# Optimization experiments

Measured on AMD Instinct MI355X. Metric: run time of the kernel, lower is better.

Reference implementation:

```python
import jax, jax.numpy as jnp
import numpy as np

E, S, Q, NN_NODES, R = 2048, 256, 25, 36, 15
H = 128  # MLP hidden width


def setup_inputs() -> dict:
    key = jax.random.key(0)
    ks = jax.random.split(key, 16)
    g = lambda k, shape, scale=1.0: (jax.random.normal(k, shape, dtype=jnp.float32) * scale)
    inp = {
        "nodes": g(ks[0], (E, NN_NODES, 2)),
        "W1": g(ks[1], (2, H), 1.0 / np.sqrt(2.0)),
        "b1": jnp.zeros((H,), jnp.float32),
        "W2": g(ks[2], (H, H), 1.0 / np.sqrt(H)),
        "b2": jnp.zeros((H,), jnp.float32),
        "W3": g(ks[3], (H, H), 1.0 / np.sqrt(H)),
        "b3": jnp.zeros((H,), jnp.float32),
        "W4": g(ks[4], (H, 1), 1.0 / np.sqrt(H)),
        "b4": jnp.zeros((1,), jnp.float32),
        # 2nd-derivative interpolation matrices of the inter basis B at the
        # sub-element quadrature points (shared across big elements).
        "Ixx": g(ks[5], (S, Q, NN_NODES), 0.1),
        "Iyy": g(ks[6], (S, Q, NN_NODES), 0.1),
        # per-big-element 2x2 Hessian change-of-coordinates map (B_DD_inter)
        "B_DD": g(ks[7], (E, 2, 2)),
        "w_quad": jax.random.uniform(ks[8], (Q,), dtype=jnp.float32),
        # test-function values at quadrature points (b.Base)
        "Base": g(ks[9], (Q, R)),
        # per-sub-element Jacobians and precomputed RHS projections F_total
        "J": jax.random.uniform(ks[10], (E, S), dtype=jnp.float32),
        "F": g(ks[11], (E, S, R)),
    }
    return inp


def _mlp(x, W1, b1, W2, b2, W3, b3, W4, b4):
    h = jnp.tanh(x @ W1 + b1)
    h = jnp.tanh(h @ W2 + b2)
    h = jnp.tanh(h @ W3 + b3)
    return h @ W4 + b4


def reference(nodes, W1, b1, W2, b2, W3, b3, W4, b4,
              Ixx, Iyy, B_DD, w_quad, Base, J, F):
    # NN evaluated once per big element at its interpolation nodes: [E, n_nodes]
    ev = _mlp(nodes.reshape(-1, 2), W1, b1, W2, b2, W3, b3, W4, b4)
    ev = ev.reshape(E, NN_NODES)
    d2x = jnp.einsum("sqn,en->esq", Ixx, ev)
    d2y = jnp.einsum("sqn,en->esq", Iyy, ev)
    grad_second = jnp.stack([d2x, d2y], axis=2)           # [E,S,2,Q]
    # B_DD_inter @ grad_second^T, per big element
    grad_second = jnp.einsum("eij,esjq->esiq", B_DD, grad_second)
    integrand_1 = grad_second.sum(axis=2)                 # [E,S,Q]
    # u_NN_el[r] = -J * sum_q w[q] * Base[q,r] * integrand_1[q]
    u_el = -J[:, :, None] * jnp.einsum("q,qr,esq->esr", w_quad, Base, integrand_1)
    res = u_el - F                                        # [E,S,R]
    # loss_element = mean over test functions, summed over all (big, sub) elements
    return jnp.sum(jnp.mean(jnp.square(res), axis=-1))
```

## Files before the change

### kernel.cpp

```cpp
#include <hip/hip_runtime.h>

#define EN 2048
#define SN 256
#define QN 25
#define NNODES 36
#define RN 15
#define HN 128
#define KP 96
#define NTOT (SN * RN)

typedef __attribute__((ext_vector_type(8))) short short8;
typedef __attribute__((ext_vector_type(4))) float f32x4;
typedef __attribute__((ext_vector_type(2))) unsigned int uint2v;

__device__ __forceinline__ unsigned short f2bf(float f) {
    unsigned int u = __float_as_uint(f);
    u += 0x7fffu + ((u >> 16) & 1u);
    return (unsigned short)(u >> 16);
}
__device__ __forceinline__ float bf2f(unsigned short h) {
    return __uint_as_float(((unsigned int)h) << 16);
}
__device__ __forceinline__ float fast_tanh(float x) {
    float xs = x * 2.885390082f;
    xs = fminf(fmaxf(xs, -60.f), 60.f);
    float e = __builtin_amdgcn_exp2f(xs);
    float r = __builtin_amdgcn_rcpf(e + 1.f);
    return fmaf(-2.f, r, 1.f);
}

__device__ __forceinline__ void load_W(const float* __restrict__ W,
                                       unsigned short (*Ws)[136], int t)
{
    const int n = t & 127;
    const int h = t >> 7;
    #pragma unroll
    for (int kk = 0; kk < 16; kk++) {
        const int k0 = (kk * 2 + h) * 4;
        const float a0 = W[(k0 + 0) * HN + n];
        const float a1 = W[(k0 + 1) * HN + n];
        const float a2 = W[(k0 + 2) * HN + n];
        const float a3 = W[(k0 + 3) * HN + n];
        uint2v pk;
        pk[0] = (unsigned)f2bf(a0) | ((unsigned)f2bf(a1) << 16);
        pk[1] = (unsigned)f2bf(a2) | ((unsigned)f2bf(a3) << 16);
        *(uint2v*)&Ws[n][k0] = pk;
    }
}

__device__ __forceinline__ void mfma_layer(unsigned short (*Hs)[136],
                                           const unsigned short (*Ws)[136],
                                           const float* __restrict__ bias,
                                           int wv, int rowA, int quad)
{
    const int r0 = wv * 32;
    short8 afrag[2][4];
    #pragma unroll
    for (int rt = 0; rt < 2; rt++)
        #pragma unroll
        for (int kt = 0; kt < 4; kt++)
            afrag[rt][kt] = *(const short8*)&Hs[r0 + rt * 16 + rowA][kt * 32 + quad * 8];

    f32x4 acc[2][8];
    const f32x4 zero = {0.f, 0.f, 0.f, 0.f};
    #pragma unroll
    for (int rt = 0; rt < 2; rt++)
        #pragma unroll
        for (int nt = 0; nt < 8; nt++) acc[rt][nt] = zero;

    #pragma unroll
    for (int nt = 0; nt < 8; nt++) {
        #pragma unroll
        for (int kt = 0; kt < 4; kt++) {
            const short8 bfrag = *(const short8*)&Ws[nt * 16 + rowA][kt * 32 + quad * 8];
            acc[0][nt] = __builtin_amdgcn_mfma_f32_16x16x32_bf16(afrag[0][kt], bfrag, acc[0][nt], 0, 0, 0);
            acc[1][nt] = __builtin_amdgcn_mfma_f32_16x16x32_bf16(afrag[1][kt], bfrag, acc[1][nt], 0, 0, 0);
        }
    }
    #pragma unroll
    for (int nt = 0; nt < 8; nt++) {
        const int col = nt * 16 + rowA;
        const float bv = bias[col];
        #pragma unroll
        for (int rt = 0; rt < 2; rt++) {
            #pragma unroll
            for (int rg = 0; rg < 4; rg++) {
                const float v = fast_tanh(acc[rt][nt][rg] + bv);
                Hs[r0 + rt * 16 + quad * 4 + rg][col] = f2bf(v);
            }
        }
    }
}

#define MLP_BLOCKS 576
#define MC_BLOCKS  SN

__global__ __launch_bounds__(256, 2)
void prep_kernel(const float* __restrict__ nodes,
                 const float* __restrict__ W1, const float* __restrict__ b1,
                 const float* __restrict__ W2, const float* __restrict__ b2,
                 const float* __restrict__ W3, const float* __restrict__ b3,
                 const float* __restrict__ W4, const float* __restrict__ b4,
                 const float* __restrict__ B_DD,
                 const float* __restrict__ Ixx, const float* __restrict__ Iyy,
                 const float* __restrict__ wq, const float* __restrict__ Base,
                 unsigned short* __restrict__ evcb,
                 unsigned short* __restrict__ Mcb,
                 float* __restrict__ out)
{
    __shared__ unsigned short Hs[128][136];
    __shared__ unsigned short Ws[128][136];
    __shared__ float WB[QN * 16];
    const int bid = blockIdx.x;
    const int t   = threadIdx.x;

    if (bid < MLP_BLOCKS) {
        const int lane = t & 63;
        const int wv   = t >> 6;
        const int rowA = lane & 15;
        const int quad = lane >> 4;

        {
            const int p  = t >> 1;
            const int P  = bid * 128 + p;
            const float x0 = nodes[2 * P], x1 = nodes[2 * P + 1];
            const int n0 = (t & 1) * 64;
            #pragma unroll
            for (int i = 0; i < 16; i++) {
                const int n = n0 + 4 * i;
                const float4 wa = *(const float4*)(W1 + n);
                const float4 wb = *(const float4*)(W1 + HN + n);
                const float4 bb = *(const float4*)(b1 + n);
                const float h0 = fast_tanh(fmaf(x0, wa.x, fmaf(x1, wb.x, bb.x)));
                const float h1 = fast_tanh(fmaf(x0, wa.y, fmaf(x1, wb.y, bb.y)));
                const float h2 = fast_tanh(fmaf(x0, wa.z, fmaf(x1, wb.z, bb.z)));
                const float h3 = fast_tanh(fmaf(x0, wa.w, fmaf(x1, wb.w, bb.w)));
                uint2v pk;
                pk[0] = (unsigned)f2bf(h0) | ((unsigned)f2bf(h1) << 16);
                pk[1] = (unsigned)f2bf(h2) | ((unsigned)f2bf(h3) << 16);
                *(uint2v*)&Hs[p][n] = pk;
            }
        }
        load_W(W2, Ws, t);
        __syncthreads();
        mfma_layer(Hs, Ws, b2, wv, rowA, quad);
        __syncthreads();
        load_W(W3, Ws, t);
        __syncthreads();
        mfma_layer(Hs, Ws, b3, wv, rowA, quad);
        {
            const int p  = t >> 1;
            const int k0 = (t & 1) * 64;
            float d = 0.f;
            #pragma unroll
            for (int i = 0; i < 8; i++) {
                const short8 h = *(const short8*)&Hs[p][k0 + 8 * i];
                const float4 wA = *(const float4*)(W4 + k0 + 8 * i);
                const float4 wB = *(const float4*)(W4 + k0 + 8 * i + 4);
                d = fmaf(bf2f((unsigned short)h[0]), wA.x, d);
                d = fmaf(bf2f((unsigned short)h[1]), wA.y, d);
                d = fmaf(bf2f((unsigned short)h[2]), wA.z, d);
                d = fmaf(bf2f((unsigned short)h[3]), wA.w, d);
                d = fmaf(bf2f((unsigned short)h[4]), wB.x, d);
                d = fmaf(bf2f((unsigned short)h[5]), wB.y, d);
                d = fmaf(bf2f((unsigned short)h[6]), wB.z, d);
                d = fmaf(bf2f((unsigned short)h[7]), wB.w, d);
            }
            d += __shfl_xor(d, 1, 64);
            if ((t & 1) == 0) {
                const float ev = d + b4[0];
                const int P  = bid * 128 + p;
                const int e  = P / NNODES;
                const int ne = P - e * NNODES;
                const float c0 = B_DD[4 * e + 0] + B_DD[4 * e + 2];
                const float c1 = B_DD[4 * e + 1] + B_DD[4 * e + 3];
                evcb[e * KP + ne]          = f2bf(c0 * ev);
                evcb[e * KP + NNODES + ne] = f2bf(c1 * ev);
                if (ne < KP - 2 * NNODES)
                    evcb[e * KP + 2 * NNODES + ne] = 0;
            }
        }
    } else {
        const int s = bid - MLP_BLOCKS;
        if (s == 0 && t == 0) out[0] = 0.f;
        float* I_lds = (float*)&Hs[0][0];
        for (int i = t; i < QN * 16; i += 256) {
            const int q = i >> 4, r = i & 15;
            if (r < RN) WB[i] = wq[q] * Base[q * RN + r];
        }
        const float* __restrict__ Ia = Ixx + (size_t)s * (QN * NNODES);
        const float* __restrict__ Ib = Iyy + (size_t)s * (QN * NNODES);
        for (int i = t; i < QN * NNODES; i += 256) {
            I_lds[i]               = Ia[i];
            I_lds[QN * NNODES + i] = Ib[i];
        }
        __syncthreads();
        for (int o = t; o < RN * KP; o += 256) {
            const int c = o % KP;
            const int r = o / KP;
            float v = 0.f;
            if (c < 2 * NNODES) {
                const float* __restrict__ Ip =
                    I_lds + ((c < NNODES) ? c : (QN * NNODES + c - NNODES));
                float a0 = 0.f, a1 = 0.f;
                #pragma unroll
                for (int q = 0; q < QN - 1; q += 2) {
                    a0 = fmaf(WB[q * 16 + r],       Ip[q * NNODES],       a0);
                    a1 = fmaf(WB[(q + 1) * 16 + r], Ip[(q + 1) * NNODES], a1);
                }
                a0 = fmaf(WB[(QN - 1) * 16 + r], Ip[(QN - 1) * NNODES], a0);
                v = a0 + a1;
            }
            Mcb[((size_t)s * RN + r) * KP + c] = f2bf(v);
        }
    }
}

__global__ __launch_bounds__(256, 4)
void loss_kernel(const unsigned short* __restrict__ evcb,
                 const unsigned short* __restrict__ Mcb,
                 const float* __restrict__ J, const float* __restrict__ F,
                 float* __restrict__ out)
{
    const int t    = threadIdx.x;
    const int lane = t & 63;
    const int wv   = t >> 6;
    const int rowA = lane & 15;
    const int quad = lane >> 4;
    const int m0 = (blockIdx.x & 31) * 64;
    const int n0 = (blockIdx.x >> 5) * 128 + wv * 32;

    float Fv[2][16];
    #pragma unroll
    for (int nt = 0; nt < 2; nt++) {
        const int n = n0 + nt * 16 + rowA;
        #pragma unroll
        for (int mt = 0; mt < 4; mt++)
            #pragma unroll
            for (int rg = 0; rg < 4; rg++)
                Fv[nt][mt * 4 + rg] = F[(size_t)(m0 + mt * 16 + quad * 4 + rg) * NTOT + n];
    }

    f32x4 acc[4][2];
    const f32x4 zero = {0.f, 0.f, 0.f, 0.f};
    #pragma unroll
    for (int mt = 0; mt < 4; mt++)
        #pragma unroll
        for (int nt = 0; nt < 2; nt++) acc[mt][nt] = zero;

    #pragma unroll
    for (int kt = 0; kt < 3; kt++) {
        short8 a[4], b[2];
        #pragma unroll
        for (int mt = 0; mt < 4; mt++)
            a[mt] = *(const short8*)&evcb[(size_t)(m0 + mt * 16 + rowA) * KP + kt * 32 + quad * 8];
        #pragma unroll
        for (int nt = 0; nt < 2; nt++)
            b[nt] = *(const short8*)&Mcb[(size_t)(n0 + nt * 16 + rowA) * KP + kt * 32 + quad * 8];
        #pragma unroll
        for (int mt = 0; mt < 4; mt++)
            #pragma unroll
            for (int nt = 0; nt < 2; nt++)
                acc[mt][nt] = __builtin_amdgcn_mfma_f32_16x16x32_bf16(a[mt], b[nt], acc[mt][nt], 0, 0, 0);
    }

    float total = 0.f;
    #pragma unroll
    for (int nt = 0; nt < 2; nt++) {
        const int n = n0 + nt * 16 + rowA;
        const int s = (n * 34953) >> 19;
        #pragma unroll
        for (int mt = 0; mt < 4; mt++) {
            const int eb = m0 + mt * 16 + quad * 4;
            #pragma unroll
            for (int rg = 0; rg < 4; rg++) {
                const float Jv = J[(size_t)(eb + rg) * SN + s];
                const float d  = acc[mt][nt][rg];
                const float res = fmaf(-Jv, d, -Fv[nt][mt * 4 + rg]);
                total = fmaf(res, res, total);
            }
        }
    }
    total *= (1.f / (float)RN);

    #pragma unroll
    for (int off = 32; off; off >>= 1)
        total += __shfl_down(total, off, 64);
    __shared__ float wsum[4];
    if (lane == 0) wsum[wv] = total;
    __syncthreads();
    if (t == 0) atomicAdd(out, (wsum[0] + wsum[1]) + (wsum[2] + wsum[3]));
}

extern "C" void kernel_launch(void* const* d_in, const int* in_sizes, int n_in,
                              void* d_out, int out_size, void* d_ws, size_t ws_size,
                              hipStream_t stream)
{
    (void)in_sizes; (void)n_in; (void)out_size; (void)ws_size;
    const float* nodes = (const float*)d_in[0];
    const float* W1   = (const float*)d_in[1];
    const float* b1   = (const float*)d_in[2];
    const float* W2   = (const float*)d_in[3];
    const float* b2   = (const float*)d_in[4];
    const float* W3   = (const float*)d_in[5];
    const float* b3   = (const float*)d_in[6];
    const float* W4   = (const float*)d_in[7];
    const float* b4   = (const float*)d_in[8];
    const float* Ixx  = (const float*)d_in[9];
    const float* Iyy  = (const float*)d_in[10];
    const float* B_DD = (const float*)d_in[11];
    const float* wq   = (const float*)d_in[12];
    const float* Base = (const float*)d_in[13];
    const float* J    = (const float*)d_in[14];
    const float* F    = (const float*)d_in[15];
    float* out = (float*)d_out;
    unsigned short* evcb = (unsigned short*)d_ws;
    unsigned short* Mcb  = (unsigned short*)((char*)d_ws + EN * KP * 2);

    prep_kernel<<<MLP_BLOCKS + MC_BLOCKS, 256, 0, stream>>>(
        nodes, W1, b1, W2, b2, W3, b3, W4, b4, B_DD, Ixx, Iyy, wq, Base,
        evcb, Mcb, out);
    loss_kernel<<<32 * 30, 256, 0, stream>>>(evcb, Mcb, J, F, out);
}
```

Before: 145.8 us.

## Prefetch F and J into cache during prep, reorder block roles, drop tanh clamp

The M-matrix blocks are moved to the front of the prep grid, and after computing their Mcb slice they stream all of F and J through loads whose results are kept live but discarded. The goal is to warm the large last-level cache so that loss_kernel's reads of F and J hit cache instead of HBM, overlapping that traffic with the MLP blocks. The clamp in fast_tanh is also removed, which saves two instructions per activation but relies on exp2 overflowing to inf and rcp of inf giving 0. The extra prefetch pass adds about 32MB of reads to the prep kernel and only helps if the data is still cached when loss_kernel runs.

```diff
diff --git a/kernel.cpp b/kernel.cpp
--- a/kernel.cpp
+++ b/kernel.cpp
@@ -22,9 +22,7 @@
     return __uint_as_float(((unsigned int)h) << 16);
 }
 __device__ __forceinline__ float fast_tanh(float x) {
-    float xs = x * 2.885390082f;
-    xs = fminf(fmaxf(xs, -60.f), 60.f);
-    float e = __builtin_amdgcn_exp2f(xs);
+    float e = __builtin_amdgcn_exp2f(x * 2.885390082f);
     float r = __builtin_amdgcn_rcpf(e + 1.f);
     return fmaf(-2.f, r, 1.f);
 }
@@ -92,8 +90,8 @@
     }
 }
 
+#define MC_BLOCKS  SN
 #define MLP_BLOCKS 576
-#define MC_BLOCKS  SN
 
 __global__ __launch_bounds__(256, 2)
 void prep_kernel(const float* __restrict__ nodes,
@@ -104,6 +102,7 @@
                  const float* __restrict__ B_DD,
                  const float* __restrict__ Ixx, const float* __restrict__ Iyy,
                  const float* __restrict__ wq, const float* __restrict__ Base,
+                 const float* __restrict__ Fin, const float* __restrict__ Jin,
                  unsigned short* __restrict__ evcb,
                  unsigned short* __restrict__ Mcb,
                  float* __restrict__ out)
@@ -114,7 +113,8 @@
     const int bid = blockIdx.x;
     const int t   = threadIdx.x;
 
-    if (bid < MLP_BLOCKS) {
+    if (bid >= MC_BLOCKS) {
+        const int mb   = bid - MC_BLOCKS;
         const int lane = t & 63;
         const int wv   = t >> 6;
         const int rowA = lane & 15;
@@ -122,7 +122,7 @@
 
         {
             const int p  = t >> 1;
-            const int P  = bid * 128 + p;
+            const int P  = mb * 128 + p;
             const float x0 = nodes[2 * P], x1 = nodes[2 * P + 1];
             const int n0 = (t & 1) * 64;
             #pragma unroll
@@ -169,7 +169,7 @@
             d += __shfl_xor(d, 1, 64);
             if ((t & 1) == 0) {
                 const float ev = d + b4[0];
-                const int P  = bid * 128 + p;
+                const int P  = mb * 128 + p;
                 const int e  = P / NNODES;
                 const int ne = P - e * NNODES;
                 const float c0 = B_DD[4 * e + 0] + B_DD[4 * e + 2];
@@ -181,7 +181,7 @@
             }
         }
     } else {
-        const int s = bid - MLP_BLOCKS;
+        const int s = bid;
         if (s == 0 && t == 0) out[0] = 0.f;
         float* I_lds = (float*)&Hs[0][0];
         for (int i = t; i < QN * 16; i += 256) {
@@ -212,6 +212,22 @@
                 v = a0 + a1;
             }
             Mcb[((size_t)s * RN + r) * KP + c] = f2bf(v);
+        }
+        {
+            const size_t base = (size_t)s * 256 + t;
+            const size_t stride = (size_t)MC_BLOCKS * 256;
+            const float4* F4 = (const float4*)Fin;
+            const size_t nF4 = (size_t)EN * NTOT / 4;
+            for (size_t i = base; i < nF4; i += stride) {
+                float4 v = F4[i];
+                asm volatile("" :: "v"(v.x), "v"(v.y), "v"(v.z), "v"(v.w));
+            }
+            const float4* J4 = (const float4*)Jin;
+            const size_t nJ4 = (size_t)EN * SN / 4;
+            for (size_t i = base; i < nJ4; i += stride) {
+                float4 v = J4[i];
+                asm volatile("" :: "v"(v.x), "v"(v.y), "v"(v.z), "v"(v.w));
+            }
         }
     }
 }
@@ -317,8 +333,8 @@
     unsigned short* evcb = (unsigned short*)d_ws;
     unsigned short* Mcb  = (unsigned short*)((char*)d_ws + EN * KP * 2);
 
-    prep_kernel<<<MLP_BLOCKS + MC_BLOCKS, 256, 0, stream>>>(
+    prep_kernel<<<MC_BLOCKS + MLP_BLOCKS, 256, 0, stream>>>(
         nodes, W1, b1, W2, b2, W3, b3, W4, b4, B_DD, Ixx, Iyy, wq, Base,
-        evcb, Mcb, out);
+        F, J, evcb, Mcb, out);
     loss_kernel<<<32 * 30, 256, 0, stream>>>(evcb, Mcb, J, F, out);
 }
```

Result: no change. 146.4 us (+0.4%).
